# Optimization experiments

Hardware: AMD Instinct MI355X
Metric: run time of the kernel (lower is better)

Reference implementation:

```python
import jax, jax.numpy as jnp
import numpy as np

N = 50000   # nodes
E = 800000  # edges (avg degree 16)
D = 128     # hidden_channels
L = 4       # num_layers
ALPHA = 0.1


def setup_inputs() -> dict:
    key = jax.random.key(0)
    ks = jax.random.split(key, 6)
    x = jax.random.normal(ks[0], (N, D), dtype=jnp.float32)
    w = jax.random.uniform(ks[1], (E,), dtype=jnp.float32)
    src = jax.random.randint(ks[2], (E,), 0, N)
    dst = jax.random.randint(ks[3], (E,), 0, N)
    # stacked per-layer Linear params
    W = jax.random.normal(ks[4], (L, D, D), dtype=jnp.float32) / np.float32(np.sqrt(D))
    b = jax.random.normal(ks[5], (L, D), dtype=jnp.float32) * 0.01
    # GPR coefficients: alpha*(1-alpha)^k, last = (1-alpha)^L
    temp_np = ALPHA * (1 - ALPHA) ** np.arange(L + 1)
    temp_np[-1] = (1 - ALPHA) ** L
    temp = jnp.asarray(temp_np, dtype=jnp.float32)
    return {"x": x, "w": w, "src": src, "dst": dst, "W": W, "b": b, "temp": temp}


def reference(x, w, src, dst, W, b, temp):
    # eval mode: dropout / dropout_adj are no-ops; edge_attn=False
    hidden = x * temp[0]
    for i in range(L):
        h = x @ W[i] + b[i]                 # [N, D] linear
        msg = h[src] * w[:, None]           # gather + edge-weight, [E, D]
        x = jax.ops.segment_sum(msg, dst, num_segments=N)  # scatter-sum
        x = jax.nn.relu(x)
        hidden = hidden + x * temp[i + 1]
    return hidden
```

## Files before the change

### kernel.cpp

```cpp
#include <hip/hip_runtime.h>
#include <hip/hip_fp16.h>

#define N_NODES 50000
#define N_EDGES 800000
#define DIM 128
#define LAYERS 4
#define SLOT 48
#define EPB 8

#define PACK_BLOCKS 782
#define WT_BLOCKS 256
#define INIT_BLOCKS 3125
#define BUCKET_BLOCKS 3128

typedef __attribute__((ext_vector_type(8))) _Float16 half8;
typedef __attribute__((ext_vector_type(4))) float float4v;
typedef __attribute__((ext_vector_type(2))) float float2v;
typedef __attribute__((ext_vector_type(8))) unsigned short ushort8;

__device__ __forceinline__ int pack_edge(int s, float w) {
    return (int)(((unsigned)__half_as_ushort(__float2half(w)) << 16) | (unsigned)(s & 0xFFFF));
}

__device__ __forceinline__ void fp8x8_to_f32(uint2 v, float* f) {
    float2v a = __builtin_amdgcn_cvt_pk_f32_fp8(v.x, false);
    float2v b = __builtin_amdgcn_cvt_pk_f32_fp8(v.x, true);
    float2v c = __builtin_amdgcn_cvt_pk_f32_fp8(v.y, false);
    float2v d = __builtin_amdgcn_cvt_pk_f32_fp8(v.y, true);
    f[0] = a[0]; f[1] = a[1]; f[2] = b[0]; f[3] = b[1];
    f[4] = c[0]; f[5] = c[1]; f[6] = d[0]; f[7] = d[1];
}

__device__ __forceinline__ uint2 f32x8_to_fp8(const float* f) {
    unsigned lo = 0, hi = 0;
    lo = __builtin_amdgcn_cvt_pk_fp8_f32(f[0], f[1], lo, false);
    lo = __builtin_amdgcn_cvt_pk_fp8_f32(f[2], f[3], lo, true);
    hi = __builtin_amdgcn_cvt_pk_fp8_f32(f[4], f[5], hi, false);
    hi = __builtin_amdgcn_cvt_pk_fp8_f32(f[6], f[7], hi, true);
    return make_uint2(lo, hi);
}

__global__ __launch_bounds__(256) void prep1_kernel(const int* __restrict__ src,
                                                    const int* __restrict__ dst,
                                                    const float* __restrict__ w,
                                                    unsigned short* __restrict__ dst16,
                                                    int* __restrict__ epk,
                                                    const float* __restrict__ W,
                                                    __half* __restrict__ Wt,
                                                    const float4* __restrict__ x,
                                                    uint2* __restrict__ xh0) {
    int bid = blockIdx.x;
    int tid = threadIdx.x;
    if (bid < PACK_BLOCKS) {
        int e = (bid * 256 + tid) * 4;
        if (e >= N_EDGES) return;
        int4   d4 = *(const int4*)(dst + e);
        int4   s4 = *(const int4*)(src + e);
        float4 w4 = *(const float4*)(w + e);
        uint2 dd;
        dd.x = ((unsigned)d4.x & 0xFFFF) | ((unsigned)d4.y << 16);
        dd.y = ((unsigned)d4.z & 0xFFFF) | ((unsigned)d4.w << 16);
        *(uint2*)(dst16 + e) = dd;
        int4 pk = make_int4(pack_edge(s4.x, w4.x), pack_edge(s4.y, w4.y),
                            pack_edge(s4.z, w4.z), pack_edge(s4.w, w4.w));
        *(int4*)(epk + e) = pk;
    } else if (bid < PACK_BLOCKS + WT_BLOCKS) {
        int i = (bid - PACK_BLOCKS) * 256 + tid;
        int l   = i >> 14;
        int rem = i & 16383;
        int k = rem >> 7;
        int n = rem & 127;
        Wt[(size_t)l * DIM * DIM + n * DIM + k] =
            __float2half(W[(size_t)l * DIM * DIM + k * DIM + n]);
    } else {
        int i = (bid - PACK_BLOCKS - WT_BLOCKS) * 256 + tid;
        float4 a = x[(size_t)i * 2];
        float4 b = x[(size_t)i * 2 + 1];
        float f[8] = { a.x, a.y, a.z, a.w, b.x, b.y, b.z, b.w };
        xh0[i] = f32x8_to_fp8(f);
    }
}

__device__ __forceinline__ void bucket_one(int d, int pk, int g,
                                           int* __restrict__ cnt,
                                           int* __restrict__ edge_buf) {
    if ((d & 7) == g) {
        int pos = atomicAdd(&cnt[d], 1);
        edge_buf[(size_t)d * SLOT + pos] = pk;
    }
}

__global__ __launch_bounds__(256) void bucket_kernel(const unsigned short* __restrict__ dst16,
                                                     const int* __restrict__ epk,
                                                     int* __restrict__ cnt,
                                                     int* __restrict__ edge_buf) {
    int g     = blockIdx.x & 7;
    int chunk = blockIdx.x >> 3;
    int base  = (chunk * 256 + threadIdx.x) * EPB;
    if (base >= N_EDGES) return;
    ushort8 d8 = *(const ushort8*)(dst16 + base);
    int4    pa = *(const int4*)(epk + base);
    int4    pb = *(const int4*)(epk + base + 4);
    bucket_one(d8[0], pa.x, g, cnt, edge_buf);
    bucket_one(d8[1], pa.y, g, cnt, edge_buf);
    bucket_one(d8[2], pa.z, g, cnt, edge_buf);
    bucket_one(d8[3], pa.w, g, cnt, edge_buf);
    bucket_one(d8[4], pb.x, g, cnt, edge_buf);
    bucket_one(d8[5], pb.y, g, cnt, edge_buf);
    bucket_one(d8[6], pb.z, g, cnt, edge_buf);
    bucket_one(d8[7], pb.w, g, cnt, edge_buf);
}

__device__ __forceinline__ void batch8(const uint2* __restrict__ x8,
                                       int m, int base, int cnt_r, int r, int c,
                                       float* accf, float& wsum) {
    uint2 v[8]; float wv[8];
    #pragma unroll
    for (int u = 0; u < 8; ++u) {
        int jj = base + u;
        int p  = __shfl(m, (r << 4) | (jj & 15), 64);
        bool live = (jj < cnt_r);
        wv[u] = live
                  ? __half2float(__ushort_as_half((unsigned short)((unsigned)p >> 16)))
                  : 0.f;
        uint2 vv = make_uint2(0u, 0u);
        if (live) vv = x8[(size_t)(p & 0xFFFF) * 16 + c];
        v[u] = vv;
    }
    #pragma unroll
    for (int u = 0; u < 8; ++u) {
        wsum += wv[u];
        float f[8];
        fp8x8_to_f32(v[u], f);
        #pragma unroll
        for (int t = 0; t < 8; ++t)
            accf[t] += wv[u] * f[t];
    }
}

#define AP 136
template <bool FINAL>
__global__ __launch_bounds__(256) void layer_kernel(const uint2* __restrict__ xin8,
                                                    const int* __restrict__ cnt_arr,
                                                    const int* __restrict__ edge_buf,
                                                    const __half* __restrict__ Wt,
                                                    const float* __restrict__ bl,
                                                    uint2* __restrict__ xout,
                                                    float* __restrict__ hidden,
                                                    const float* __restrict__ temp,
                                                    const uint2* __restrict__ x0h,
                                                    const uint2* __restrict__ x1h,
                                                    const uint2* __restrict__ x2h) {
    __shared__ __half Ah[16][AP];
    __shared__ float winS[16];
    int tid  = threadIdx.x;
    int wave = tid >> 6;
    int lane = tid & 63;
    int r = lane >> 4;
    int c = lane & 15;
    int node0  = blockIdx.x * 16 + wave * 4;
    int node_r = node0 + r;

    size_t mb = (size_t)node_r * SLOT;
    int m0 = edge_buf[mb + c];
    int m1 = edge_buf[mb + 16 + c];
    int4 c4 = *(const int4*)(cnt_arr + node0);

    int cnt_r = (r == 0) ? c4.x : (r == 1) ? c4.y : (r == 2) ? c4.z : c4.w;
    int maxc  = max(max(c4.x, c4.y), max(c4.z, c4.w));

    float accf[8];
    #pragma unroll
    for (int t = 0; t < 8; ++t) accf[t] = 0.f;
    float wsum = 0.f;

    batch8(xin8, m0, 0, cnt_r, r, c, accf, wsum);
    batch8(xin8, m0, 8, cnt_r, r, c, accf, wsum);
    if (maxc > 16) {
        batch8(xin8, m1, 16, cnt_r, r, c, accf, wsum);
        batch8(xin8, m1, 24, cnt_r, r, c, accf, wsum);
    }
    if (maxc > 32) {
        int m2 = edge_buf[mb + 32 + c];
        batch8(xin8, m2, 32, cnt_r, r, c, accf, wsum);
        batch8(xin8, m2, 40, cnt_r, r, c, accf, wsum);
    }

    union { __half2 hh[4]; float4 f4; } ua;
    ua.hh[0] = __floats2half2_rn(accf[0], accf[1]);
    ua.hh[1] = __floats2half2_rn(accf[2], accf[3]);
    ua.hh[2] = __floats2half2_rn(accf[4], accf[5]);
    ua.hh[3] = __floats2half2_rn(accf[6], accf[7]);
    int lr = wave * 4 + r;
    *(float4*)&Ah[lr][c * 8] = ua.f4;
    if (c == 0) winS[lr] = wsum;
    __syncthreads();

    int am  = lane & 15;
    int ak8 = (lane >> 4) * 8;
    float4v acc0 = (float4v)(0.f), acc1 = (float4v)(0.f);
    #pragma unroll
    for (int kk = 0; kk < 4; ++kk) {
        int k0 = kk * 32 + ak8;
        half8 a  = *(const half8*)&Ah[am][k0];
        half8 b0 = *(const half8*)(Wt + (size_t)(wave * 32 + am) * DIM + k0);
        half8 b1 = *(const half8*)(Wt + (size_t)(wave * 32 + 16 + am) * DIM + k0);
        acc0 = __builtin_amdgcn_mfma_f32_16x16x32_f16(a, b0, acc0, 0, 0, 0);
        acc1 = __builtin_amdgcn_mfma_f32_16x16x32_f16(a, b1, acc1, 0, 0, 0);
    }
    __syncthreads();

    int q  = lane >> 4;
    int cc = lane & 15;
    {
        int col = wave * 32 + cc;
        float bv = bl[col];
        #pragma unroll
        for (int j = 0; j < 4; ++j) {
            int row = q * 4 + j;
            Ah[row][col] = __float2half(fmaxf(acc0[j] + winS[row] * bv, 0.f));
        }
        col = wave * 32 + 16 + cc;
        bv = bl[col];
        #pragma unroll
        for (int j = 0; j < 4; ++j) {
            int row = q * 4 + j;
            Ah[row][col] = __float2half(fmaxf(acc1[j] + winS[row] * bv, 0.f));
        }
    }
    __syncthreads();

    int row = tid >> 4;
    int ch  = tid & 15;
    int gnode = blockIdx.x * 16 + row;
    half8 hv = *(const half8*)&Ah[row][ch * 8];
    size_t ro = (size_t)gnode * 16 + ch;

    if constexpr (!FINAL) {
        float f[8];
        #pragma unroll
        for (int t = 0; t < 8; ++t) f[t] = (float)hv[t];
        xout[ro] = f32x8_to_fp8(f);
    } else {
        float t0 = temp[0], t1 = temp[1], t2 = temp[2], t3 = temp[3], t4 = temp[4];
        uint2 u0 = x0h[ro], u1 = x1h[ro], u2 = x2h[ro], u3 = xin8[ro];
        float f0[8], f1[8], f2[8], f3[8];
        fp8x8_to_f32(u0, f0);
        fp8x8_to_f32(u1, f1);
        fp8x8_to_f32(u2, f2);
        fp8x8_to_f32(u3, f3);
        float out[8];
        #pragma unroll
        for (int t = 0; t < 8; ++t)
            out[t] = t0 * f0[t] + t1 * f1[t] + t2 * f2[t]
                   + t3 * f3[t] + t4 * (float)hv[t];
        size_t o = (size_t)gnode * DIM + ch * 8;
        *(float4*)(hidden + o)     = make_float4(out[0], out[1], out[2], out[3]);
        *(float4*)(hidden + o + 4) = make_float4(out[4], out[5], out[6], out[7]);
    }
}

extern "C" void kernel_launch(void* const* d_in, const int* in_sizes, int n_in,
                              void* d_out, int out_size, void* d_ws, size_t ws_size,
                              hipStream_t stream) {
    const float* x    = (const float*)d_in[0];
    const float* w    = (const float*)d_in[1];
    const int*   src  = (const int*)d_in[2];
    const int*   dst  = (const int*)d_in[3];
    const float* W    = (const float*)d_in[4];
    const float* b    = (const float*)d_in[5];
    const float* temp = (const float*)d_in[6];
    float* hidden = (float*)d_out;

    char* ws = (char*)d_ws;
    uint2* X0 = (uint2*)ws;                  ws += (size_t)N_NODES * DIM;
    uint2* X1 = (uint2*)ws;                  ws += (size_t)N_NODES * DIM;
    uint2* X2 = (uint2*)ws;                  ws += (size_t)N_NODES * DIM;
    uint2* X3 = (uint2*)ws;                  ws += (size_t)N_NODES * DIM;
    __half* Wt = (__half*)ws;                ws += (size_t)LAYERS * DIM * DIM * sizeof(__half);
    int* cnt = (int*)ws;                     ws += (size_t)N_NODES * sizeof(int);
    int* edge_buf = (int*)ws;                ws += (size_t)(N_NODES * SLOT + 64) * sizeof(int);
    unsigned short* dst16 = (unsigned short*)ws;  ws += (size_t)N_EDGES * sizeof(unsigned short);
    int* epk = (int*)ws;                     ws += (size_t)N_EDGES * sizeof(int);

    hipMemsetAsync(cnt, 0, (size_t)N_NODES * sizeof(int), stream);
    prep1_kernel<<<PACK_BLOCKS + WT_BLOCKS + INIT_BLOCKS, 256, 0, stream>>>(
        src, dst, w, dst16, epk, W, Wt, (const float4*)x, X0);
    bucket_kernel<<<BUCKET_BLOCKS, 256, 0, stream>>>(dst16, epk, cnt, edge_buf);

    const int layer_blocks = N_NODES / 16;
    layer_kernel<false><<<layer_blocks, 256, 0, stream>>>(
        X0, cnt, edge_buf, Wt + 0 * DIM * DIM, b + 0 * DIM,
        X1, hidden, temp, nullptr, nullptr, nullptr);
    layer_kernel<false><<<layer_blocks, 256, 0, stream>>>(
        X1, cnt, edge_buf, Wt + 1 * DIM * DIM, b + 1 * DIM,
        X2, hidden, temp, nullptr, nullptr, nullptr);
    layer_kernel<false><<<layer_blocks, 256, 0, stream>>>(
        X2, cnt, edge_buf, Wt + 2 * DIM * DIM, b + 2 * DIM,
        X3, hidden, temp, nullptr, nullptr, nullptr);
    layer_kernel<true><<<layer_blocks, 256, 0, stream>>>(
        X3, cnt, edge_buf, Wt + 3 * DIM * DIM, b + 3 * DIM,
        nullptr, hidden, temp, X0, X1, X2);
}
```

Before: 249.8 us.

## Fold count zeroing into prep kernel and widen bucket and gather batches

Replaces the separate memset of the per-node counters with extra blocks inside the prep kernel, which removes one launch. The bucket kernel now handles 16 edges per thread with half as many blocks. The layer gather issues 16 neighbour loads per batch instead of 8 to raise memory-level parallelism. The wider batches raise register pressure and do more masked loads for low-degree nodes.

```diff
diff --git a/kernel.cpp b/kernel.cpp
--- a/kernel.cpp
+++ b/kernel.cpp
@@ -6,12 +6,13 @@
 #define DIM 128
 #define LAYERS 4
 #define SLOT 48
-#define EPB 8
+#define EPB 16
 
 #define PACK_BLOCKS 782
 #define WT_BLOCKS 256
 #define INIT_BLOCKS 3125
-#define BUCKET_BLOCKS 3128
+#define CNT_BLOCKS 196
+#define BUCKET_BLOCKS 1568
 
 typedef __attribute__((ext_vector_type(8))) _Float16 half8;
 typedef __attribute__((ext_vector_type(4))) float float4v;
@@ -48,7 +49,8 @@
                                                     const float* __restrict__ W,
                                                     __half* __restrict__ Wt,
                                                     const float4* __restrict__ x,
-                                                    uint2* __restrict__ xh0) {
+                                                    uint2* __restrict__ xh0,
+                                                    int* __restrict__ cnt) {
     int bid = blockIdx.x;
     int tid = threadIdx.x;
     if (bid < PACK_BLOCKS) {
@@ -72,12 +74,15 @@
         int n = rem & 127;
         Wt[(size_t)l * DIM * DIM + n * DIM + k] =
             __float2half(W[(size_t)l * DIM * DIM + k * DIM + n]);
-    } else {
+    } else if (bid < PACK_BLOCKS + WT_BLOCKS + INIT_BLOCKS) {
         int i = (bid - PACK_BLOCKS - WT_BLOCKS) * 256 + tid;
         float4 a = x[(size_t)i * 2];
         float4 b = x[(size_t)i * 2 + 1];
         float f[8] = { a.x, a.y, a.z, a.w, b.x, b.y, b.z, b.w };
         xh0[i] = f32x8_to_fp8(f);
+    } else {
+        int i = (bid - PACK_BLOCKS - WT_BLOCKS - INIT_BLOCKS) * 256 + tid;
+        if (i < N_NODES) cnt[i] = 0;
     }
 }
 
@@ -98,25 +103,36 @@
     int chunk = blockIdx.x >> 3;
     int base  = (chunk * 256 + threadIdx.x) * EPB;
     if (base >= N_EDGES) return;
-    ushort8 d8 = *(const ushort8*)(dst16 + base);
-    int4    pa = *(const int4*)(epk + base);
-    int4    pb = *(const int4*)(epk + base + 4);
-    bucket_one(d8[0], pa.x, g, cnt, edge_buf);
-    bucket_one(d8[1], pa.y, g, cnt, edge_buf);
-    bucket_one(d8[2], pa.z, g, cnt, edge_buf);
-    bucket_one(d8[3], pa.w, g, cnt, edge_buf);
-    bucket_one(d8[4], pb.x, g, cnt, edge_buf);
-    bucket_one(d8[5], pb.y, g, cnt, edge_buf);
-    bucket_one(d8[6], pb.z, g, cnt, edge_buf);
-    bucket_one(d8[7], pb.w, g, cnt, edge_buf);
-}
-
-__device__ __forceinline__ void batch8(const uint2* __restrict__ x8,
-                                       int m, int base, int cnt_r, int r, int c,
-                                       float* accf, float& wsum) {
-    uint2 v[8]; float wv[8];
+    ushort8 d8a = *(const ushort8*)(dst16 + base);
+    ushort8 d8b = *(const ushort8*)(dst16 + base + 8);
+    int4 p0 = *(const int4*)(epk + base);
+    int4 p1 = *(const int4*)(epk + base + 4);
+    int4 p2 = *(const int4*)(epk + base + 8);
+    int4 p3 = *(const int4*)(epk + base + 12);
+    bucket_one(d8a[0], p0.x, g, cnt, edge_buf);
+    bucket_one(d8a[1], p0.y, g, cnt, edge_buf);
+    bucket_one(d8a[2], p0.z, g, cnt, edge_buf);
+    bucket_one(d8a[3], p0.w, g, cnt, edge_buf);
+    bucket_one(d8a[4], p1.x, g, cnt, edge_buf);
+    bucket_one(d8a[5], p1.y, g, cnt, edge_buf);
+    bucket_one(d8a[6], p1.z, g, cnt, edge_buf);
+    bucket_one(d8a[7], p1.w, g, cnt, edge_buf);
+    bucket_one(d8b[0], p2.x, g, cnt, edge_buf);
+    bucket_one(d8b[1], p2.y, g, cnt, edge_buf);
+    bucket_one(d8b[2], p2.z, g, cnt, edge_buf);
+    bucket_one(d8b[3], p2.w, g, cnt, edge_buf);
+    bucket_one(d8b[4], p3.x, g, cnt, edge_buf);
+    bucket_one(d8b[5], p3.y, g, cnt, edge_buf);
+    bucket_one(d8b[6], p3.z, g, cnt, edge_buf);
+    bucket_one(d8b[7], p3.w, g, cnt, edge_buf);
+}
+
+__device__ __forceinline__ void batch16(const uint2* __restrict__ x8,
+                                        int m, int base, int cnt_r, int r, int c,
+                                        float* accf, float& wsum) {
+    uint2 v[16]; float wv[16];
     #pragma unroll
-    for (int u = 0; u < 8; ++u) {
+    for (int u = 0; u < 16; ++u) {
         int jj = base + u;
         int p  = __shfl(m, (r << 4) | (jj & 15), 64);
         bool live = (jj < cnt_r);
@@ -128,7 +144,7 @@
         v[u] = vv;
     }
     #pragma unroll
-    for (int u = 0; u < 8; ++u) {
+    for (int u = 0; u < 16; ++u) {
         wsum += wv[u];
         float f[8];
         fp8x8_to_f32(v[u], f);
@@ -174,16 +190,12 @@
     for (int t = 0; t < 8; ++t) accf[t] = 0.f;
     float wsum = 0.f;
 
-    batch8(xin8, m0, 0, cnt_r, r, c, accf, wsum);
-    batch8(xin8, m0, 8, cnt_r, r, c, accf, wsum);
-    if (maxc > 16) {
-        batch8(xin8, m1, 16, cnt_r, r, c, accf, wsum);
-        batch8(xin8, m1, 24, cnt_r, r, c, accf, wsum);
-    }
+    batch16(xin8, m0, 0, cnt_r, r, c, accf, wsum);
+    if (maxc > 16)
+        batch16(xin8, m1, 16, cnt_r, r, c, accf, wsum);
     if (maxc > 32) {
         int m2 = edge_buf[mb + 32 + c];
-        batch8(xin8, m2, 32, cnt_r, r, c, accf, wsum);
-        batch8(xin8, m2, 40, cnt_r, r, c, accf, wsum);
+        batch16(xin8, m2, 32, cnt_r, r, c, accf, wsum);
     }
 
     union { __half2 hh[4]; float4 f4; } ua;
@@ -283,9 +295,8 @@
     unsigned short* dst16 = (unsigned short*)ws;  ws += (size_t)N_EDGES * sizeof(unsigned short);
     int* epk = (int*)ws;                     ws += (size_t)N_EDGES * sizeof(int);
 
-    hipMemsetAsync(cnt, 0, (size_t)N_NODES * sizeof(int), stream);
-    prep1_kernel<<<PACK_BLOCKS + WT_BLOCKS + INIT_BLOCKS, 256, 0, stream>>>(
-        src, dst, w, dst16, epk, W, Wt, (const float4*)x, X0);
+    prep1_kernel<<<PACK_BLOCKS + WT_BLOCKS + INIT_BLOCKS + CNT_BLOCKS, 256, 0, stream>>>(
+        src, dst, w, dst16, epk, W, Wt, (const float4*)x, X0, cnt);
     bucket_kernel<<<BUCKET_BLOCKS, 256, 0, stream>>>(dst16, epk, cnt, edge_buf);
 
     const int layer_blocks = N_NODES / 16;
```

Result: slower. 263.1 us (+5.4%).
